# Kernel tuning notes

Measured on AMD Instinct MI355X. Metric: run time of the kernel, lower is better.

## Reference

```python
import jax, jax.numpy as jnp
import numpy as np

NUM_HEADS = 12
HEAD_DIM = 64
DROPKEY = 0.1
BN_EPS = 1e-5


def setup_inputs() -> dict:
    key = jax.random.key(0)
    ks = jax.random.split(key, 6)
    b, n, d = 4, 1024, 768
    img_c, hw = 256, 32
    x = jax.random.normal(ks[0], (b, n, d), dtype=jnp.float32)
    y = jax.random.normal(ks[1], (b, img_c, hw, hw), dtype=jnp.float32)
    drop_mask = jax.random.uniform(ks[2], (b, NUM_HEADS, n, n), dtype=jnp.float32)
    W_qkv = jax.random.normal(ks[3], (d, 3 * d), dtype=jnp.float32) * (d ** -0.5)
    conv1_w = jax.random.normal(ks[4], (img_c, 1, 3, 3), dtype=jnp.float32) * 0.1
    conv2_w = jax.random.normal(ks[5], (d, img_c, 1, 1), dtype=jnp.float32) * (img_c ** -0.5)
    bn_gamma = jnp.ones((d,), dtype=jnp.float32)
    bn_beta = jnp.zeros((d,), dtype=jnp.float32)
    return {"x": x, "y": y, "drop_mask": drop_mask, "W_qkv": W_qkv,
            "conv1_w": conv1_w, "conv2_w": conv2_w,
            "bn_gamma": bn_gamma, "bn_beta": bn_beta}


def reference(x, y, drop_mask, W_qkv, conv1_w, conv2_w, bn_gamma, bn_beta):
    b, n, d = x.shape
    h, hd = NUM_HEADS, HEAD_DIM
    scale = hd ** -0.5

    # --- attention branch ---
    qkv = x @ W_qkv                                     # [b, n, 3d]
    q, k, v = jnp.split(qkv, 3, axis=-1)
    def to_heads(t):
        return t.reshape(b, n, h, hd).transpose(0, 2, 1, 3)  # [b, h, n, hd]
    q, k, v = to_heads(q), to_heads(k), to_heads(v)
    scores = jnp.einsum('bhid,bhjd->bhij', q, k) * scale
    # dropkey: bernoulli(p) additive -1e12 mask before softmax
    mask = (drop_mask < DROPKEY).astype(scores.dtype)
    scores = scores + mask * jnp.asarray(-1e12, scores.dtype)
    attn = jax.nn.softmax(scores, axis=-1)
    out = jnp.einsum('bhij,bhjd->bhid', attn, v)        # [b, h, n, hd]
    out = out.transpose(0, 2, 1, 3).reshape(b, n, h * hd)

    # --- conv branch: depthwise 3x3 -> 1x1 -> BN(train) -> ReLU ---
    img_c = y.shape[1]
    y1 = jax.lax.conv_general_dilated(
        y, conv1_w, window_strides=(1, 1), padding='SAME',
        dimension_numbers=('NCHW', 'OIHW', 'NCHW'),
        feature_group_count=img_c)                      # [b, img_c, H, W]
    y2 = jax.lax.conv_general_dilated(
        y1, conv2_w, window_strides=(1, 1), padding='SAME',
        dimension_numbers=('NCHW', 'OIHW', 'NCHW'))     # [b, d, H, W]
    mean = jnp.mean(y2, axis=(0, 2, 3), keepdims=True)
    var = jnp.var(y2, axis=(0, 2, 3), keepdims=True)
    y_bn = (y2 - mean) * jax.lax.rsqrt(var + BN_EPS)
    y_bn = y_bn * bn_gamma[None, :, None, None] + bn_beta[None, :, None, None]
    y_out = jax.nn.relu(y_bn)                           # [b, d, H, W]

    # patchify(p1=p2=1) + flatten == 'b c h w -> b (h w) c'
    y_tok = y_out.transpose(0, 2, 3, 1).reshape(b, n, d)
    return (out + y_tok, y_out)


if __name__ == '__main__':
    inp = setup_inputs()
    o, yo = jax.jit(reference)(**inp)
    print(o.shape, yo.shape)
```

## Files before the change

kernel.cpp:

```cpp
#include <hip/hip_runtime.h>
#include <cstddef>

#define B_     4
#define NTOK   1024
#define DMODEL 768
#define NH     12
#define IMGC   256
#define NPIX   1024

typedef __attribute__((ext_vector_type(8))) short bf16x8;
typedef __attribute__((ext_vector_type(4))) float f32x4;
typedef __attribute__((ext_vector_type(8))) unsigned short u16x8;

static __device__ __forceinline__ unsigned short f2bf(float f) {
  unsigned int u = __float_as_uint(f);
  u += 0x7FFFu + ((u >> 16) & 1u);
  return (unsigned short)(u >> 16);
}

#define SWZ(row, b) (((row) << 7) + ((b) ^ (((row) & 7) << 4)))

#define GLOAD16(g, l) __builtin_amdgcn_global_load_lds(                      \
    (const __attribute__((address_space(1))) void*)(g),                      \
    (__attribute__((address_space(3))) void*)(l), 16, 0, 0)

__global__ __launch_bounds__(256) void k_cvt(const float* __restrict__ X,
                                             const float* __restrict__ Wqkv,
                                             const float* __restrict__ W2,
                                             const float* __restrict__ Yimg,
                                             const float* __restrict__ w1,
                                             unsigned short* __restrict__ Xb,
                                             unsigned short* __restrict__ Wtb,
                                             unsigned short* __restrict__ W2b,
                                             float* __restrict__ y1,
                                             float* __restrict__ bnacc) {
  __shared__ unsigned short T[32][33];
  const int bid = blockIdx.x;
  const int t = threadIdx.x;
  if (bid < 1536) {
    const size_t i8 = (size_t)bid * 256 + t;
    const float4 a = *(const float4*)(X + i8 * 8);
    const float4 b = *(const float4*)(X + i8 * 8 + 4);
    u16x8 o;
    o[0] = f2bf(a.x); o[1] = f2bf(a.y); o[2] = f2bf(a.z); o[3] = f2bf(a.w);
    o[4] = f2bf(b.x); o[5] = f2bf(b.y); o[6] = f2bf(b.z); o[7] = f2bf(b.w);
    *(u16x8*)(Xb + i8 * 8) = o;
  } else if (bid < 3264) {
    const int b2 = bid - 1536;
    const int n0 = (b2 % 72) * 32, k0 = (b2 / 72) * 32;
    const int tx = t & 31, ty = t >> 5;
#pragma unroll
    for (int i = 0; i < 4; i++) {
      int kl = ty + i * 8;
      T[tx][kl] = f2bf(Wqkv[(size_t)(k0 + kl) * 2304 + n0 + tx]);
    }
    __syncthreads();
#pragma unroll
    for (int i = 0; i < 4; i++) {
      int nl = ty + i * 8;
      Wtb[(size_t)(n0 + nl) * 768 + k0 + tx] = T[nl][tx];
    }
  } else if (bid < 3360) {
    const size_t i8 = (size_t)(bid - 3264) * 256 + t;
    const float4 a = *(const float4*)(W2 + i8 * 8);
    const float4 b = *(const float4*)(W2 + i8 * 8 + 4);
    u16x8 o;
    o[0] = f2bf(a.x); o[1] = f2bf(a.y); o[2] = f2bf(a.z); o[3] = f2bf(a.w);
    o[4] = f2bf(b.x); o[5] = f2bf(b.y); o[6] = f2bf(b.z); o[7] = f2bf(b.w);
    *(u16x8*)(W2b + i8 * 8) = o;
  } else if (bid == 3360) {
    for (int i = t; i < 1536; i += 256) bnacc[i] = 0.0f;
  } else {
    const int bc = bid - 3361;
    const int c = bc & 255;
    const float* yin = Yimg + (size_t)bc * NPIX;
    float* yout = y1 + (size_t)bc * NPIX;
    float w[9];
#pragma unroll
    for (int i = 0; i < 9; i++) w[i] = w1[c * 9 + i];
#pragma unroll
    for (int rep = 0; rep < 4; rep++) {
      int px = t + rep * 256;
      int yy = px >> 5, xx = px & 31;
      float acc = 0.0f;
#pragma unroll
      for (int dy = -1; dy <= 1; dy++) {
        int sy = yy + dy;
        if (sy < 0 || sy > 31) continue;
#pragma unroll
        for (int dx = -1; dx <= 1; dx++) {
          int sx = xx + dx;
          if (sx < 0 || sx > 31) continue;
          acc = fmaf(yin[(sy << 5) + sx], w[(dy + 1) * 3 + dx + 1], acc);
        }
      }
      yout[px] = acc;
    }
  }
}

__global__ __launch_bounds__(256) void k_trans(const float* __restrict__ y1,
                                               unsigned short* __restrict__ y1t) {
  __shared__ float T[64][65];
  const int p0 = blockIdx.x * 64, c0 = blockIdx.y * 64, b = blockIdx.z;
  const int t = threadIdx.x;
  const float* src = y1 + ((size_t)b << 18);
  {
    const int pl = t & 63, cl0 = t >> 6;
#pragma unroll
    for (int i = 0; i < 16; i++) {
      int cl = cl0 * 16 + i;
      T[cl][pl] = src[(size_t)(c0 + cl) * 1024 + p0 + pl];
    }
  }
  __syncthreads();
  {
    const int cl = t & 63, pl0 = t >> 6;
    unsigned short* dst = y1t + ((size_t)b << 18);
#pragma unroll
    for (int i = 0; i < 16; i++) {
      int pl = pl0 * 16 + i;
      dst[(size_t)(p0 + pl) * 256 + c0 + cl] = f2bf(T[cl][pl]);
    }
  }
}

__global__ __launch_bounds__(256) void k_mm(const unsigned short* __restrict__ Xb,
                                            const unsigned short* __restrict__ Wt,
                                            unsigned short* __restrict__ q,
                                            unsigned short* __restrict__ k,
                                            unsigned short* __restrict__ v,
                                            const unsigned short* __restrict__ W2b,
                                            const unsigned short* __restrict__ y1t,
                                            float* __restrict__ Y2,
                                            float* __restrict__ bn_sum,
                                            float* __restrict__ bn_sumsq) {
  __shared__ __align__(16) char AsB[16384];
  __shared__ __align__(16) char BsB[16384];
  const int bid = blockIdx.x;
  const int t = threadIdx.x;
  const int w = t >> 6, l = t & 63;
  const int r = l & 15, g = l >> 4;
  const int wr = w >> 1, wc = w & 1;
  const int rsel  = l >> 3;
  const int slotp = (l & 7) ^ (rsel & 7);
  f32x4 acc[4][4] = {};

  if (bid < 576) {
    const int bx = bid % 18, by = bid / 18;
    const int m0 = by * 128;
    const int n0 = bx * 128;
    for (int step = 0; step < 12; ++step) {
      const int k0 = step * 64;
#pragma unroll
      for (int i = 0; i < 4; i++) {
        const int chunk = (i << 2) + w;
        const int row = (chunk << 3) + rsel;
        GLOAD16(Xb + (size_t)(m0 + row) * 768 + k0 + (slotp << 3),
                AsB + (chunk << 10) + (l << 4));
        GLOAD16(Wt + (size_t)(n0 + row) * 768 + k0 + (slotp << 3),
                BsB + (chunk << 10) + (l << 4));
      }
      __syncthreads();
#pragma unroll
      for (int kk = 0; kk < 2; kk++) {
        bf16x8 a[4], b[4];
#pragma unroll
        for (int m = 0; m < 4; m++) {
          const int row = wr * 64 + m * 16 + r;
          a[m] = *(const bf16x8*)(AsB + SWZ(row, kk * 64 + (g << 4)));
        }
#pragma unroll
        for (int n = 0; n < 4; n++) {
          const int row = wc * 64 + n * 16 + r;
          b[n] = *(const bf16x8*)(BsB + SWZ(row, kk * 64 + (g << 4)));
        }
#pragma unroll
        for (int m = 0; m < 4; m++)
#pragma unroll
          for (int n = 0; n < 4; n++)
            acc[m][n] = __builtin_amdgcn_mfma_f32_16x16x32_bf16(a[m], b[n], acc[m][n], 0, 0, 0);
      }
      __syncthreads();
    }
    const int which = bx / 6;
    const int cbase = (bx - which * 6) * 128 + wc * 64;
    unsigned short* dst = which == 0 ? q : (which == 1 ? k : v);
#pragma unroll
    for (int m = 0; m < 4; m++) {
      const int grow = m0 + wr * 64 + m * 16 + g * 4;
#pragma unroll
      for (int n = 0; n < 4; n++) {
        const int c = cbase + n * 16 + r;
        const int head = c >> 6, dim = c & 63;
#pragma unroll
        for (int reg = 0; reg < 4; reg++) {
          const int row = grow + reg;
          const int bb = row >> 10, tok = row & 1023;
          dst[((size_t)(((bb * NH + head) << 10) + tok) << 6) + dim] = f2bf(acc[m][n][reg]);
        }
      }
    }
  } else {
    const int b2 = bid - 576;
    const int n0 = (b2 & 7) * 128;
    const int m0 = ((b2 >> 3) % 6) * 128;
    const int b  = b2 / 48;
    const unsigned short* Bb = y1t + ((size_t)b << 18);
    for (int step = 0; step < 4; ++step) {
      const int k0 = step * 64;
#pragma unroll
      for (int i = 0; i < 4; i++) {
        const int chunk = (i << 2) + w;
        const int row = (chunk << 3) + rsel;
        GLOAD16(W2b + (size_t)(m0 + row) * 256 + k0 + (slotp << 3),
                AsB + (chunk << 10) + (l << 4));
        GLOAD16(Bb + (size_t)(n0 + row) * 256 + k0 + (slotp << 3),
                BsB + (chunk << 10) + (l << 4));
      }
      __syncthreads();
#pragma unroll
      for (int kk = 0; kk < 2; kk++) {
        bf16x8 a[4], bfr[4];
#pragma unroll
        for (int m = 0; m < 4; m++) {
          const int row = wr * 64 + m * 16 + r;
          a[m] = *(const bf16x8*)(AsB + SWZ(row, kk * 64 + (g << 4)));
        }
#pragma unroll
        for (int n = 0; n < 4; n++) {
          const int row = wc * 64 + n * 16 + r;
          bfr[n] = *(const bf16x8*)(BsB + SWZ(row, kk * 64 + (g << 4)));
        }
#pragma unroll
        for (int m = 0; m < 4; m++)
#pragma unroll
          for (int n = 0; n < 4; n++)
            acc[m][n] = __builtin_amdgcn_mfma_f32_16x16x32_bf16(a[m], bfr[n], acc[m][n], 0, 0, 0);
      }
      __syncthreads();
    }
    float* Yb = Y2 + (((size_t)b * DMODEL) << 10);
#pragma unroll
    for (int m = 0; m < 4; m++) {
#pragma unroll
      for (int reg = 0; reg < 4; reg++) {
        const int oc = m0 + wr * 64 + m * 16 + g * 4 + reg;
        float s = 0.0f, sq = 0.0f;
#pragma unroll
        for (int n = 0; n < 4; n++) {
          const int p = n0 + wc * 64 + n * 16 + r;
          const float val = acc[m][n][reg];
          Yb[((size_t)oc << 10) + p] = val;
          s += val;
          sq = fmaf(val, val, sq);
        }
        s  += __shfl_xor(s, 1);  sq += __shfl_xor(sq, 1);
        s  += __shfl_xor(s, 2);  sq += __shfl_xor(sq, 2);
        s  += __shfl_xor(s, 4);  sq += __shfl_xor(sq, 4);
        s  += __shfl_xor(s, 8);  sq += __shfl_xor(sq, 8);
        if (r == 0) {
          atomicAdd(&bn_sum[oc], s);
          atomicAdd(&bn_sumsq[oc], sq);
        }
      }
    }
  }
}

__global__ __launch_bounds__(256) void k_attn(const unsigned short* __restrict__ qb,
                                              const unsigned short* __restrict__ kb,
                                              const unsigned short* __restrict__ vb,
                                              const float* __restrict__ dm,
                                              const float* __restrict__ y2,
                                              const float* __restrict__ bn_sum,
                                              const float* __restrict__ bn_sumsq,
                                              const float* __restrict__ gamma,
                                              const float* __restrict__ beta,
                                              float* __restrict__ out0,
                                              float* __restrict__ out1) {
  __shared__ __align__(16) unsigned short QsA[4096];
  __shared__ __align__(16) unsigned short KsA[4096];
  __shared__ __align__(16) unsigned short VtA[4096];
  __shared__ __align__(16) unsigned short PsA[4096];
  const int bid = blockIdx.x;
  const int t  = threadIdx.x;
  if (bid >= 768) {
    const int row = bid - 768;
    const int c = row % DMODEL;
    const float S = bn_sum[c], SQ = bn_sumsq[c];
    const float mean = S * (1.0f / 4096.0f);
    const float var = SQ * (1.0f / 4096.0f) - mean * mean;
    const float rstd = rsqrtf(var + 1e-5f);
    const float sc = gamma[c] * rstd;
    const float sh = fmaf(-mean, sc, beta[c]);
    const float* src = y2 + ((size_t)row << 10) + t * 4;
    float* dst = out1 + ((size_t)row << 10) + t * 4;
    float4 vv = *(const float4*)src;
    vv.x = fmaxf(fmaf(vv.x, sc, sh), 0.0f);
    vv.y = fmaxf(fmaf(vv.y, sc, sh), 0.0f);
    vv.z = fmaxf(fmaf(vv.z, sc, sh), 0.0f);
    vv.w = fmaxf(fmaf(vv.w, sc, sh), 0.0f);
    *(float4*)dst = vv;
    return;
  }
  char* qs = (char*)QsA; char* ks = (char*)KsA;
  char* vt = (char*)VtA; char* ps = (char*)PsA;
  const int bh = bid % 48;
  const int qt = bid / 48;
  const int w = t >> 6, l = t & 63, r = l & 15, g = l >> 4;
  const size_t hbase = (size_t)bh << 16;
  const char* qg = (const char*)(qb + hbase + ((size_t)qt << 12));
  const char* kg = (const char*)(kb + hbase);
  const char* vg = (const char*)(vb + hbase);
  const float* mp = dm + ((size_t)bh << 20) + ((size_t)(qt * 64) << 10);

#pragma unroll
  for (int i = 0; i < 2; i++) {
    int cid = t + (i << 8);
    int row = cid >> 3, slot = cid & 7;
    uint4 val = *(const uint4*)(qg + row * 128 + slot * 16);
    *(uint4*)(qs + SWZ(row, slot * 16)) = val;
  }

  float m_run[4] = {-INFINITY, -INFINITY, -INFINITY, -INFINITY};
  float l_run[4] = {0.0f, 0.0f, 0.0f, 0.0f};
  f32x4 O[4] = {};

  for (int kt = 0; kt < 16; kt++) {
    __syncthreads();
#pragma unroll
    for (int i = 0; i < 2; i++) {
      int cid = t + (i << 8);
      int row = cid >> 3, slot = cid & 7;
      uint4 val = *(const uint4*)(kg + (size_t)(kt * 64 + row) * 128 + slot * 16);
      *(uint4*)(ks + SWZ(row, slot * 16)) = val;
    }
    {
      int j = t & 63, dh = t >> 6;
      const char* vrow = vg + (size_t)(kt * 64 + j) * 128 + dh * 32;
      u16x8 v0 = *(const u16x8*)(vrow);
      u16x8 v1 = *(const u16x8*)(vrow + 16);
#pragma unroll
      for (int e = 0; e < 8; e++) {
        *(unsigned short*)(vt + SWZ(dh * 16 + e, 2 * j))     = v0[e];
        *(unsigned short*)(vt + SWZ(dh * 16 + 8 + e, 2 * j)) = v1[e];
      }
    }
    float md[4][4];
    {
      const float* mr = mp + (size_t)(w * 16 + g * 4) * 1024 + kt * 64 + r;
#pragma unroll
      for (int reg = 0; reg < 4; reg++)
#pragma unroll
        for (int jt = 0; jt < 4; jt++)
          md[reg][jt] = mr[reg * 1024 + jt * 16];
    }
    __syncthreads();

    f32x4 s[4] = {};
    bf16x8 aQ[2];
#pragma unroll
    for (int kc = 0; kc < 2; kc++)
      aQ[kc] = *(const bf16x8*)(qs + SWZ(w * 16 + r, kc * 64 + g * 16));
#pragma unroll
    for (int jt = 0; jt < 4; jt++) {
#pragma unroll
      for (int kc = 0; kc < 2; kc++) {
        bf16x8 bK = *(const bf16x8*)(ks + SWZ(jt * 16 + r, kc * 64 + g * 16));
        s[jt] = __builtin_amdgcn_mfma_f32_16x16x32_bf16(aQ[kc], bK, s[jt], 0, 0, 0);
      }
    }
    float sv[4][4];
#pragma unroll
    for (int jt = 0; jt < 4; jt++)
#pragma unroll
      for (int reg = 0; reg < 4; reg++)
        sv[jt][reg] = s[jt][reg] * 0.125f + (md[reg][jt] < 0.1f ? -1e12f : 0.0f);

    float alpha[4];
#pragma unroll
    for (int reg = 0; reg < 4; reg++) {
      float mt = fmaxf(fmaxf(sv[0][reg], sv[1][reg]), fmaxf(sv[2][reg], sv[3][reg]));
      mt = fmaxf(mt, __shfl_xor(mt, 1));
      mt = fmaxf(mt, __shfl_xor(mt, 2));
      mt = fmaxf(mt, __shfl_xor(mt, 4));
      mt = fmaxf(mt, __shfl_xor(mt, 8));
      float mn = fmaxf(m_run[reg], mt);
      alpha[reg] = __expf(m_run[reg] - mn);
      m_run[reg] = mn;
    }
#pragma unroll
    for (int reg = 0; reg < 4; reg++) {
      int row = w * 16 + g * 4 + reg;
      float ps_ = 0.0f;
#pragma unroll
      for (int jt = 0; jt < 4; jt++) {
        float p = __expf(sv[jt][reg] - m_run[reg]);
        ps_ += p;
        *(unsigned short*)(ps + SWZ(row, 2 * (jt * 16 + r))) = f2bf(p);
      }
      ps_ += __shfl_xor(ps_, 1);
      ps_ += __shfl_xor(ps_, 2);
      ps_ += __shfl_xor(ps_, 4);
      ps_ += __shfl_xor(ps_, 8);
      l_run[reg] = l_run[reg] * alpha[reg] + ps_;
    }
#pragma unroll
    for (int dt = 0; dt < 4; dt++)
#pragma unroll
      for (int reg = 0; reg < 4; reg++)
        O[dt][reg] *= alpha[reg];
    asm volatile("s_waitcnt lgkmcnt(0)" ::: "memory");
    __builtin_amdgcn_sched_barrier(0);
#pragma unroll
    for (int kc = 0; kc < 2; kc++) {
      bf16x8 aP = *(const bf16x8*)(ps + SWZ(w * 16 + r, kc * 64 + g * 16));
#pragma unroll
      for (int dt = 0; dt < 4; dt++) {
        bf16x8 bV = *(const bf16x8*)(vt + SWZ(dt * 16 + r, kc * 64 + g * 16));
        O[dt] = __builtin_amdgcn_mfma_f32_16x16x32_bf16(aP, bV, O[dt], 0, 0, 0);
      }
    }
  }
  const int bb = bh / NH, hh = bh % NH;
  float inv[4];
#pragma unroll
  for (int reg = 0; reg < 4; reg++) inv[reg] = 1.0f / l_run[reg];
  float scv[4], shv[4];
#pragma unroll
  for (int dt = 0; dt < 4; dt++) {
    const int c = hh * 64 + dt * 16 + r;
    const float S = bn_sum[c], SQ = bn_sumsq[c];
    const float mean = S * (1.0f / 4096.0f);
    const float var = SQ * (1.0f / 4096.0f) - mean * mean;
    const float rstd = rsqrtf(var + 1e-5f);
    const float sc = gamma[c] * rstd;
    scv[dt] = sc;
    shv[dt] = fmaf(-mean, sc, beta[c]);
  }
  const int prow = qt * 64 + w * 16 + g * 4;
  const float* y2p = y2 + (((size_t)(bb * DMODEL + hh * 64 + r)) << 10) + prow;
  float4 yq[4];
#pragma unroll
  for (int dt = 0; dt < 4; dt++)
    yq[dt] = *(const float4*)(y2p + ((size_t)dt << 14));
  float* op = out0 + ((size_t)(bb * 1024 + prow)) * 768 + hh * 64 + r;
#pragma unroll
  for (int reg = 0; reg < 4; reg++)
#pragma unroll
    for (int dt = 0; dt < 4; dt++) {
      const float yv = (&yq[dt].x)[reg];
      const float ytok = fmaxf(fmaf(yv, scv[dt], shv[dt]), 0.0f);
      op[(size_t)reg * 768 + dt * 16] = fmaf(O[dt][reg], inv[reg], ytok);
    }
}

extern "C" void kernel_launch(void* const* d_in, const int* in_sizes, int n_in,
                              void* d_out, int out_size, void* d_ws, size_t ws_size,
                              hipStream_t stream) {
  (void)in_sizes; (void)n_in; (void)out_size; (void)ws_size;
  const float* x    = (const float*)d_in[0];
  const float* y    = (const float*)d_in[1];
  const float* dm   = (const float*)d_in[2];
  const float* wqkv = (const float*)d_in[3];
  const float* w1   = (const float*)d_in[4];
  const float* w2   = (const float*)d_in[5];
  const float* gam  = (const float*)d_in[6];
  const float* bet  = (const float*)d_in[7];
  float* out0 = (float*)d_out;
  float* out1 = out0 + (size_t)B_ * NTOK * DMODEL;

  char* wsb = (char*)d_ws;
  unsigned short* Xb  = (unsigned short*)wsb;
  unsigned short* Wtb = (unsigned short*)(wsb + 6291456);
  unsigned short* W2b = (unsigned short*)(wsb + 9830400);
  unsigned short* qb  = (unsigned short*)(wsb + 10223616);
  unsigned short* kb  = (unsigned short*)(wsb + 16515072);
  unsigned short* vb  = (unsigned short*)(wsb + 22806528);
  unsigned short* y1t = (unsigned short*)(wsb + 29097984);
  float* y2 = (float*)(wsb + 31195136);
  float* y1 = (float*)(wsb + 35389440);
  float* bnacc = (float*)(wsb + 43778048);
  float* bn_sum = bnacc;
  float* bn_sumsq = bnacc + 768;

  k_cvt<<<dim3(4385), 256, 0, stream>>>(x, wqkv, w2, y, w1, Xb, Wtb, W2b, y1, bnacc);
  k_trans<<<dim3(16, 4, B_), 256, 0, stream>>>(y1, y1t);
  k_mm<<<dim3(768), 256, 0, stream>>>(Xb, Wtb, qb, kb, vb, W2b, y1t, y2, bn_sum, bn_sumsq);
  k_attn<<<dim3(3840), 256, 0, stream>>>(qb, kb, vb, dm, y2, bn_sum, bn_sumsq, gam, bet, out0, out1);
}
```

Measured before the change: 122.5 us.

## Pack dropkey mask into bitmask inside matmul kernel, read bits in attention

The float dropkey mask (about 200MB) is thresholded into a packed 1-bit-per-element array by extra blocks interleaved into the matmul launch, so the mask streaming overlaps with GEMM compute. The attention kernel then reads 32x fewer mask bytes and extracts penalty bits per lane. This moves the mask's memory traffic off the attention critical path, at the cost of an extra bitmask write/read and a larger matmul grid that competes with GEMM blocks for bandwidth and CUs.

```diff
diff --git a/kernel.cpp b/kernel.cpp
--- a/kernel.cpp
+++ b/kernel.cpp
@@ -134,11 +134,30 @@
                                             const unsigned short* __restrict__ y1t,
                                             float* __restrict__ Y2,
                                             float* __restrict__ bn_sum,
-                                            float* __restrict__ bn_sumsq) {
+                                            float* __restrict__ bn_sumsq,
+                                            const float* __restrict__ dm,
+                                            unsigned* __restrict__ mbits) {
   __shared__ __align__(16) char AsB[16384];
   __shared__ __align__(16) char BsB[16384];
   const int bid = blockIdx.x;
   const int t = threadIdx.x;
+  if (bid % 9) {
+    const int cid = (bid / 9) * 8 + (bid % 9) - 1;
+    const size_t wid = (size_t)cid * 256 + t;
+    const f32x4* src = (const f32x4*)(dm + wid * 32);
+    unsigned bits = 0;
+#pragma unroll
+    for (int kq = 0; kq < 8; kq++) {
+      f32x4 vv = __builtin_nontemporal_load(src + kq);
+      bits |= (unsigned)(vv.x < 0.1f) << (kq * 4 + 0);
+      bits |= (unsigned)(vv.y < 0.1f) << (kq * 4 + 1);
+      bits |= (unsigned)(vv.z < 0.1f) << (kq * 4 + 2);
+      bits |= (unsigned)(vv.w < 0.1f) << (kq * 4 + 3);
+    }
+    mbits[wid] = bits;
+    return;
+  }
+  const int gid = bid / 9;
   const int w = t >> 6, l = t & 63;
   const int r = l & 15, g = l >> 4;
   const int wr = w >> 1, wc = w & 1;
@@ -146,8 +165,8 @@
   const int slotp = (l & 7) ^ (rsel & 7);
   f32x4 acc[4][4] = {};
 
-  if (bid < 576) {
-    const int bx = bid % 18, by = bid / 18;
+  if (gid < 576) {
+    const int bx = gid % 18, by = gid / 18;
     const int m0 = by * 128;
     const int n0 = bx * 128;
     for (int step = 0; step < 12; ++step) {
@@ -202,7 +221,7 @@
       }
     }
   } else {
-    const int b2 = bid - 576;
+    const int b2 = gid - 576;
     const int n0 = (b2 & 7) * 128;
     const int m0 = ((b2 >> 3) % 6) * 128;
     const int b  = b2 / 48;
@@ -271,7 +290,7 @@
 __global__ __launch_bounds__(256) void k_attn(const unsigned short* __restrict__ qb,
                                               const unsigned short* __restrict__ kb,
                                               const unsigned short* __restrict__ vb,
-                                              const float* __restrict__ dm,
+                                              const unsigned* __restrict__ mbits,
                                               const float* __restrict__ y2,
                                               const float* __restrict__ bn_sum,
                                               const float* __restrict__ bn_sumsq,
@@ -313,7 +332,7 @@
   const char* qg = (const char*)(qb + hbase + ((size_t)qt << 12));
   const char* kg = (const char*)(kb + hbase);
   const char* vg = (const char*)(vb + hbase);
-  const float* mp = dm + ((size_t)bh << 20) + ((size_t)(qt * 64) << 10);
+  const unsigned* mbp = mbits + ((size_t)bh << 15) + (size_t)(qt * 64 + w * 16 + g * 4) * 32;
 
 #pragma unroll
   for (int i = 0; i < 2; i++) {
@@ -347,15 +366,10 @@
         *(unsigned short*)(vt + SWZ(dh * 16 + 8 + e, 2 * j)) = v1[e];
       }
     }
-    float md[4][4];
-    {
-      const float* mr = mp + (size_t)(w * 16 + g * 4) * 1024 + kt * 64 + r;
-#pragma unroll
-      for (int reg = 0; reg < 4; reg++)
-#pragma unroll
-        for (int jt = 0; jt < 4; jt++)
-          md[reg][jt] = mr[reg * 1024 + jt * 16];
-    }
+    uint2 mw[4];
+#pragma unroll
+    for (int reg = 0; reg < 4; reg++)
+      mw[reg] = *(const uint2*)(mbp + (size_t)reg * 32 + kt * 2);
     __syncthreads();
 
     f32x4 s[4] = {};
@@ -375,8 +389,11 @@
 #pragma unroll
     for (int jt = 0; jt < 4; jt++)
 #pragma unroll
-      for (int reg = 0; reg < 4; reg++)
-        sv[jt][reg] = s[jt][reg] * 0.125f + (md[reg][jt] < 0.1f ? -1e12f : 0.0f);
+      for (int reg = 0; reg < 4; reg++) {
+        const unsigned word = (jt < 2) ? mw[reg].x : mw[reg].y;
+        const float pen = ((word >> (((jt & 1) << 4) + r)) & 1) ? -1e12f : 0.0f;
+        sv[jt][reg] = fmaf(s[jt][reg], 0.125f, pen);
+      }
 
     float alpha[4];
 #pragma unroll
@@ -484,9 +501,10 @@
   float* bnacc = (float*)(wsb + 43778048);
   float* bn_sum = bnacc;
   float* bn_sumsq = bnacc + 768;
+  unsigned* mbits = (unsigned*)(wsb + 43784192);
 
   k_cvt<<<dim3(4385), 256, 0, stream>>>(x, wqkv, w2, y, w1, Xb, Wtb, W2b, y1, bnacc);
   k_trans<<<dim3(16, 4, B_), 256, 0, stream>>>(y1, y1t);
-  k_mm<<<dim3(768), 256, 0, stream>>>(Xb, Wtb, qb, kb, vb, W2b, y1t, y2, bn_sum, bn_sumsq);
-  k_attn<<<dim3(3840), 256, 0, stream>>>(qb, kb, vb, dm, y2, bn_sum, bn_sumsq, gam, bet, out0, out1);
+  k_mm<<<dim3(6912), 256, 0, stream>>>(Xb, Wtb, qb, kb, vb, W2b, y1t, y2, bn_sum, bn_sumsq, dm, mbits);
+  k_attn<<<dim3(3840), 256, 0, stream>>>(qb, kb, vb, mbits, y2, bn_sum, bn_sumsq, gam, bet, out0, out1);
 }
```

New measurement: 201.6 us. +64.6%, slower.
